# Kernel tuning notes

Measured on AMD Instinct MI355X. Metric: run time of the kernel, lower is better.

The kernel has to match this reference:

```python
import jax, jax.numpy as jnp
import numpy as np

N_LAYERS = 6
D_T = 6144   # d_transcoder (features per layer)
D_M = 768    # d_model (residual stream)
TOK = 128    # tokens (batch*seq)


def setup_inputs() -> dict:
    key = jax.random.key(0)
    k_x, k_enc, k_dec = jax.random.split(key, 3)
    x = jax.random.normal(k_x, (N_LAYERS, TOK, D_M), jnp.float32)
    W_enc = jax.random.normal(k_enc, (N_LAYERS, D_T, D_M), jnp.float32) * 0.02
    b_enc = jnp.zeros((N_LAYERS, D_T), jnp.float32)
    b_dec = jnp.zeros((N_LAYERS, D_M), jnp.float32)
    # Padded cross-layer decoder: W_dec[i, j] is the decoder from features at
    # layer i writing into layer j's MLP output; only j >= i is valid
    # (original stores a ragged list of [d_transcoder, n_layers - i, d_model]).
    W_dec = jax.random.normal(k_dec, (N_LAYERS, N_LAYERS, D_T, D_M), jnp.float32) * 0.02
    dec_mask = jnp.triu(jnp.ones((N_LAYERS, N_LAYERS), dtype=bool))  # mask[i, j] = (j >= i)
    W_dec = jnp.where(dec_mask[:, :, None, None], W_dec, 0.0)
    return {"x": x, "W_enc": W_enc, "b_enc": b_enc, "b_dec": b_dec,
            "W_dec": W_dec, "dec_mask": dec_mask}


def reference(x, W_enc, b_enc, b_dec, W_dec, dec_mask):
    # Encode: per-layer feature activations [n_layers, tok, d_transcoder]
    acts = jax.nn.relu(jnp.einsum('lnd,lfd->lnf', x, W_enc) + b_enc[:, None, :])
    # Decode: layer-i features write to all layers j >= i (mask enforces triangle)
    Wd = jnp.where(dec_mask[:, :, None, None], W_dec, 0.0)
    recon = jnp.einsum('inf,ijfd->jnd', acts, Wd) + b_dec[:, None, :]
    return recon  # [n_layers, tok, d_model]
```

## Files before the change

kernel.cpp:

```cpp
#include <hip/hip_runtime.h>
#include <hip/hip_bf16.h>

#define NL 6
#define DT 6144
#define DM 768
#define TOK 128

#define EF 32
#define EK 256
#define ENST (DM / EK)

#define TD 256
#define NTD 3
#define FC 768
#define NFC 8
#define NSTEP (FC / 32)
#define TILE_ELEMS (TOK * TD)

#define FCA 384
#define NFCA 16
#define NSTEPA (FCA / 32)

using bf16x8 = __attribute__((ext_vector_type(8))) short;
using f32x4  = __attribute__((ext_vector_type(4))) float;

typedef unsigned int u32;
typedef __attribute__((address_space(1))) const u32 gu32;
typedef __attribute__((address_space(3))) u32 lu32;

__device__ __forceinline__ void stage16(const float* g, float* l) {
  __builtin_amdgcn_global_load_lds((gu32*)g, (lu32*)l, 16, 0, 0);
}

__device__ __forceinline__ short f2bf(float f) {
  union { float f; unsigned u; } c; c.f = f;
  unsigned u = c.u;
  u += 0x7fffu + ((u >> 16) & 1u);
  return (short)(u >> 16);
}

__global__ void initcvt_k(const float* __restrict__ b_dec,
                          const float* __restrict__ x,
                          float* __restrict__ out, ushort* __restrict__ xb) {
  int idx = blockIdx.x * 256 + threadIdx.x;
  if (idx < NL * TOK * DM) {
    out[idx] = b_dec[(idx / (TOK * DM)) * DM + (idx % DM)];
    xb[idx] = (ushort)f2bf(x[idx]);
  }
}

__global__ __launch_bounds__(256, 2) void encode_k(
    const ushort* __restrict__ xb, const float* __restrict__ W_enc,
    const float* __restrict__ b_enc, ushort* __restrict__ acts)
{
  __shared__ float lw[2][EF][EK];

  const int l  = blockIdx.x / (DT / EF);
  const int f0 = (blockIdx.x % (DT / EF)) * EF;
  const int w    = threadIdx.x >> 6;
  const int lane = threadIdx.x & 63;
  const int lo = lane & 15, hi = lane >> 4;

  const float*  We = W_enc + ((size_t)l * DT + f0) * DM;
  const ushort* Xb = xb + (size_t)l * TOK * DM;

  f32x4 acc[2][2];
  #pragma unroll
  for (int mi = 0; mi < 2; ++mi)
    #pragma unroll
    for (int ni = 0; ni < 2; ++ni)
      acc[mi][ni] = f32x4{0.f, 0.f, 0.f, 0.f};

  #pragma unroll
  for (int q = 0; q < 8; ++q) {
    const int row = w * 8 + q;
    const int g   = lane ^ (row & 7);
    stage16(We + (size_t)row * DM + g * 4, &lw[0][row][0]);
  }
  __syncthreads();

  int cur = 0;
  #pragma unroll 1
  for (int st = 0; st < ENST; ++st) {
    if (st + 1 < ENST) {
      #pragma unroll
      for (int q = 0; q < 8; ++q) {
        const int row = w * 8 + q;
        const int g   = lane ^ (row & 7);
        stage16(We + (size_t)row * DM + (st + 1) * EK + g * 4,
                &lw[cur ^ 1][row][0]);
      }
    }

    const int sw = lo & 7;
    #pragma unroll
    for (int ks = 0; ks < EK / 32; ++ks) {
      bf16x8 a[2], b[2];
      #pragma unroll
      for (int mi = 0; mi < 2; ++mi)
        a[mi] = *(const bf16x8*)(Xb + (size_t)(w * 32 + mi * 16 + lo) * DM
                                 + st * EK + ks * 32 + hi * 8);
      #pragma unroll
      for (int ni = 0; ni < 2; ++ni) {
        const int c0 = (ks * 8 + hi * 2) ^ sw;
        const int c1 = (ks * 8 + hi * 2 + 1) ^ sw;
        const float4 b0 = *(const float4*)&lw[cur][ni * 16 + lo][c0 * 4];
        const float4 b1 = *(const float4*)&lw[cur][ni * 16 + lo][c1 * 4];
        b[ni][0] = f2bf(b0.x); b[ni][1] = f2bf(b0.y);
        b[ni][2] = f2bf(b0.z); b[ni][3] = f2bf(b0.w);
        b[ni][4] = f2bf(b1.x); b[ni][5] = f2bf(b1.y);
        b[ni][6] = f2bf(b1.z); b[ni][7] = f2bf(b1.w);
      }

      #pragma unroll
      for (int mi = 0; mi < 2; ++mi)
        #pragma unroll
        for (int ni = 0; ni < 2; ++ni)
          acc[mi][ni] = __builtin_amdgcn_mfma_f32_16x16x32_bf16(a[mi], b[ni], acc[mi][ni], 0, 0, 0);
    }

    __syncthreads();
    cur ^= 1;
  }

  #pragma unroll
  for (int ni = 0; ni < 2; ++ni) {
    const int f = f0 + ni * 16 + lo;
    const float bias = b_enc[l * DT + f];
    #pragma unroll
    for (int mi = 0; mi < 2; ++mi) {
      #pragma unroll
      for (int rr = 0; rr < 4; ++rr) {
        const int n = w * 32 + mi * 16 + hi * 4 + rr;
        float v = acc[mi][ni][rr] + bias;
        v = v > 0.f ? v : 0.f;
        acts[((size_t)l * TOK + n) * DT + f] = (ushort)f2bf(v);
      }
    }
  }
}

__device__ const int PI_[21]  = {0,0,0,0,0,0, 1,1,1,1,1, 2,2,2,2, 3,3,3, 4,4, 5};
__device__ const int PJ_[21]  = {0,1,2,3,4,5, 1,2,3,4,5, 2,3,4,5, 3,4,5, 4,5, 5};
__device__ const int OFFI_[6] = {0, 6, 11, 15, 18, 20};

__global__ __launch_bounds__(256, 2) void decode_part_k(
    const ushort* __restrict__ acts, const float* __restrict__ W_dec,
    float* __restrict__ part)
{
  __shared__ float lw[2][32][TD];

  const int bid = blockIdx.x;
  const int p  = bid / (NTD * NFC);
  const int rm = bid % (NTD * NFC);
  const int c  = rm / NTD;
  const int t  = rm % NTD;
  const int i = PI_[p], j = PJ_[p];
  const int w = threadIdx.x >> 6;
  const int lane = threadIdx.x & 63;
  const int lo = lane & 15, hi = lane >> 4;
  const int fb = c * FC;

  const float*  Wb = W_dec + ((size_t)(i * NL + j) * DT + fb) * DM + t * TD;
  const ushort* Ab = acts + (size_t)i * TOK * DT + fb;

  f32x4 acc[8][4];
  #pragma unroll
  for (int mi = 0; mi < 8; ++mi)
    #pragma unroll
    for (int ni = 0; ni < 4; ++ni)
      acc[mi][ni] = f32x4{0.f, 0.f, 0.f, 0.f};

  #pragma unroll
  for (int q = 0; q < 8; ++q) {
    const int row = w * 8 + q;
    stage16(Wb + (size_t)row * DM + lane * 4, &lw[0][row][0]);
  }
  __syncthreads();

  int cur = 0;
  #pragma unroll 1
  for (int s = 0; s < NSTEP; ++s) {
    if (s + 1 < NSTEP) {
      const float* Ws = Wb + (size_t)(s + 1) * 32 * DM;
      #pragma unroll
      for (int q = 0; q < 8; ++q) {
        const int row = w * 8 + q;
        stage16(Ws + (size_t)row * DM + lane * 4, &lw[cur ^ 1][row][0]);
      }
    }

    bf16x8 a[8];
    #pragma unroll
    for (int mi = 0; mi < 8; ++mi)
      a[mi] = *(const bf16x8*)(Ab + (size_t)(mi * 16 + lo) * DT + s * 32 + hi * 8);

    bf16x8 bb[4];
    #pragma unroll
    for (int ni = 0; ni < 4; ++ni) {
      const int col = w * 64 + ni * 16 + lo;
      #pragma unroll
      for (int e = 0; e < 8; ++e)
        bb[ni][e] = f2bf(lw[cur][hi * 8 + e][col]);
    }

    #pragma unroll
    for (int mi = 0; mi < 8; ++mi)
      #pragma unroll
      for (int ni = 0; ni < 4; ++ni)
        acc[mi][ni] = __builtin_amdgcn_mfma_f32_16x16x32_bf16(a[mi], bb[ni], acc[mi][ni], 0, 0, 0);

    __syncthreads();
    cur ^= 1;
  }

  float* pp = part + (size_t)bid * TILE_ELEMS;
  #pragma unroll
  for (int ni = 0; ni < 4; ++ni) {
    const int dl = w * 64 + ni * 16 + lo;
    #pragma unroll
    for (int mi = 0; mi < 8; ++mi)
      #pragma unroll
      for (int rr = 0; rr < 4; ++rr)
        pp[(size_t)(mi * 16 + hi * 4 + rr) * TD + dl] = acc[mi][ni][rr];
  }
}

__global__ void reduce_k(const float* __restrict__ part,
                         const float* __restrict__ b_dec,
                         float* __restrict__ out)
{
  const int idx = blockIdx.x * 256 + threadIdx.x;
  if (idx >= NL * TOK * DM) return;
  const int j   = idx / (TOK * DM);
  const int rem = idx % (TOK * DM);
  const int n   = rem / DM;
  const int d   = rem % DM;
  const int t   = d >> 8;
  const int dl  = d & (TD - 1);

  float s = b_dec[j * DM + d];
  for (int i = 0; i <= j; ++i) {
    const int p = OFFI_[i] + (j - i);
    const float* pb = part + ((size_t)(p * NFC) * NTD + t) * TILE_ELEMS
                      + (size_t)n * TD + dl;
    #pragma unroll
    for (int c = 0; c < NFC; ++c)
      s += pb[(size_t)c * NTD * TILE_ELEMS];
  }
  out[idx] = s;
}

__global__ __launch_bounds__(256, 2) void decode_atomic_k(
    const ushort* __restrict__ acts, const float* __restrict__ W_dec,
    float* __restrict__ out)
{
  __shared__ float lw[2][32][TD];

  const int bid = blockIdx.x;
  const int p  = bid / (NTD * NFCA);
  const int rm = bid % (NTD * NFCA);
  const int c  = rm / NTD;
  const int t  = rm % NTD;
  const int i = PI_[p], j = PJ_[p];
  const int w = threadIdx.x >> 6;
  const int lane = threadIdx.x & 63;
  const int lo = lane & 15, hi = lane >> 4;
  const int fb = c * FCA;

  const float*  Wb = W_dec + ((size_t)(i * NL + j) * DT + fb) * DM + t * TD;
  const ushort* Ab = acts + (size_t)i * TOK * DT + fb;

  f32x4 acc[8][4];
  #pragma unroll
  for (int mi = 0; mi < 8; ++mi)
    #pragma unroll
    for (int ni = 0; ni < 4; ++ni)
      acc[mi][ni] = f32x4{0.f, 0.f, 0.f, 0.f};

  #pragma unroll
  for (int q = 0; q < 8; ++q) {
    const int row = w * 8 + q;
    stage16(Wb + (size_t)row * DM + lane * 4, &lw[0][row][0]);
  }
  __syncthreads();

  int cur = 0;
  #pragma unroll 1
  for (int s = 0; s < NSTEPA; ++s) {
    if (s + 1 < NSTEPA) {
      const float* Ws = Wb + (size_t)(s + 1) * 32 * DM;
      #pragma unroll
      for (int q = 0; q < 8; ++q) {
        const int row = w * 8 + q;
        stage16(Ws + (size_t)row * DM + lane * 4, &lw[cur ^ 1][row][0]);
      }
    }

    bf16x8 a[8];
    #pragma unroll
    for (int mi = 0; mi < 8; ++mi)
      a[mi] = *(const bf16x8*)(Ab + (size_t)(mi * 16 + lo) * DT + s * 32 + hi * 8);

    bf16x8 bb[4];
    #pragma unroll
    for (int ni = 0; ni < 4; ++ni) {
      const int col = w * 64 + ni * 16 + lo;
      #pragma unroll
      for (int e = 0; e < 8; ++e)
        bb[ni][e] = f2bf(lw[cur][hi * 8 + e][col]);
    }

    #pragma unroll
    for (int mi = 0; mi < 8; ++mi)
      #pragma unroll
      for (int ni = 0; ni < 4; ++ni)
        acc[mi][ni] = __builtin_amdgcn_mfma_f32_16x16x32_bf16(a[mi], bb[ni], acc[mi][ni], 0, 0, 0);

    __syncthreads();
    cur ^= 1;
  }

  float* oj = out + (size_t)j * TOK * DM;
  #pragma unroll
  for (int ni = 0; ni < 4; ++ni) {
    const int d = t * TD + w * 64 + ni * 16 + lo;
    #pragma unroll
    for (int mi = 0; mi < 8; ++mi)
      #pragma unroll
      for (int rr = 0; rr < 4; ++rr)
        atomicAdd(oj + (size_t)(mi * 16 + hi * 4 + rr) * DM + d, acc[mi][ni][rr]);
  }
}

extern "C" void kernel_launch(void* const* d_in, const int* in_sizes, int n_in,
                              void* d_out, int out_size, void* d_ws, size_t ws_size,
                              hipStream_t stream) {
  const float* x     = (const float*)d_in[0];
  const float* W_enc = (const float*)d_in[1];
  const float* b_enc = (const float*)d_in[2];
  const float* b_dec = (const float*)d_in[3];
  const float* W_dec = (const float*)d_in[4];
  float* out = (float*)d_out;

  const size_t actsB = (size_t)NL * TOK * DT * 2;
  const size_t xbB   = (size_t)NL * TOK * DM * 2;
  const size_t partB = (size_t)21 * NFC * NTD * TILE_ELEMS * 4;

  ushort* acts = (ushort*)d_ws;
  ushort* xb   = (ushort*)((char*)d_ws + actsB);
  float*  part = (float*)((char*)d_ws + actsB + xbB);

  initcvt_k<<<dim3((NL * TOK * DM + 255) / 256), dim3(256), 0, stream>>>(b_dec, x, out, xb);
  encode_k<<<dim3(NL * (DT / EF)), dim3(256), 0, stream>>>(xb, W_enc, b_enc, acts);

  if (ws_size >= actsB + xbB + partB) {
    decode_part_k<<<dim3(21 * NFC * NTD), dim3(256), 0, stream>>>(acts, W_dec, part);
    reduce_k<<<dim3((NL * TOK * DM + 255) / 256), dim3(256), 0, stream>>>(part, b_dec, out);
  } else {
    decode_atomic_k<<<dim3(21 * NFCA * NTD), dim3(256), 0, stream>>>(acts, W_dec, out);
  }
}
```

Measured before the change: 185.1 us.

## Store decode partials in bf16, remap blocks per XCD, double encode tile per block

Decode partial sums are now written and read as bf16 instead of fp32, halving the partial buffer traffic between decode_part_k and reduce_k. Decode blocks are remapped so that consecutive logical tiles land on the same XCD (8 XCDs × 63), aiming for better L2 locality of shared acts. Each encode block now handles two 32-feature tiles in sequence (grid shrinks to NL*96), with the pipelined staging continuing across tiles. The bf16 partials lose precision in the reduction, with up to 48 partials summed per output.

```diff
diff --git a/kernel.cpp b/kernel.cpp
--- a/kernel.cpp
+++ b/kernel.cpp
@@ -9,6 +9,7 @@
 #define EF 32
 #define EK 256
 #define ENST (DM / EK)
+#define NVE (2 * ENST)
 
 #define TD 256
 #define NTD 3
@@ -37,6 +38,11 @@
   unsigned u = c.u;
   u += 0x7fffu + ((u >> 16) & 1u);
   return (short)(u >> 16);
+}
+
+__device__ __forceinline__ float bf2f(ushort u) {
+  union { unsigned u; float f; } c; c.u = ((unsigned)u) << 16;
+  return c.f;
 }
 
 __global__ void initcvt_k(const float* __restrict__ b_dec,
@@ -55,13 +61,13 @@
 {
   __shared__ float lw[2][EF][EK];
 
-  const int l  = blockIdx.x / (DT / EF);
-  const int f0 = (blockIdx.x % (DT / EF)) * EF;
+  const int l  = blockIdx.x / 96;
+  const int fp = (blockIdx.x % 96) * 64;
   const int w    = threadIdx.x >> 6;
   const int lane = threadIdx.x & 63;
   const int lo = lane & 15, hi = lane >> 4;
 
-  const float*  We = W_enc + ((size_t)l * DT + f0) * DM;
+  const float*  We = W_enc + ((size_t)l * DT + fp) * DM;
   const ushort* Xb = xb + (size_t)l * TOK * DM;
 
   f32x4 acc[2][2];
@@ -74,20 +80,23 @@
   #pragma unroll
   for (int q = 0; q < 8; ++q) {
     const int row = w * 8 + q;
-    const int g   = lane ^ (row & 7);
-    stage16(We + (size_t)row * DM + g * 4, &lw[0][row][0]);
+    stage16(We + (size_t)row * DM + (lane ^ (row & 7)) * 4, &lw[0][row][0]);
   }
   __syncthreads();
 
   int cur = 0;
   #pragma unroll 1
-  for (int st = 0; st < ENST; ++st) {
-    if (st + 1 < ENST) {
+  for (int v = 0; v < NVE; ++v) {
+    const int tt = v / ENST;
+    const int st = v % ENST;
+
+    if (v + 1 < NVE) {
+      const int tt2 = (v + 1) / ENST;
+      const int st2 = (v + 1) % ENST;
       #pragma unroll
       for (int q = 0; q < 8; ++q) {
         const int row = w * 8 + q;
-        const int g   = lane ^ (row & 7);
-        stage16(We + (size_t)row * DM + (st + 1) * EK + g * 4,
+        stage16(We + (size_t)(tt2 * EF + row) * DM + st2 * EK + (lane ^ (row & 7)) * 4,
                 &lw[cur ^ 1][row][0]);
       }
     }
@@ -119,24 +128,27 @@
           acc[mi][ni] = __builtin_amdgcn_mfma_f32_16x16x32_bf16(a[mi], b[ni], acc[mi][ni], 0, 0, 0);
     }
 
+    if (st == ENST - 1) {
+      #pragma unroll
+      for (int ni = 0; ni < 2; ++ni) {
+        const int f = fp + tt * EF + ni * 16 + lo;
+        const float bias = b_enc[l * DT + f];
+        #pragma unroll
+        for (int mi = 0; mi < 2; ++mi) {
+          #pragma unroll
+          for (int rr = 0; rr < 4; ++rr) {
+            const int n = w * 32 + mi * 16 + hi * 4 + rr;
+            float vv = acc[mi][ni][rr] + bias;
+            vv = vv > 0.f ? vv : 0.f;
+            acts[((size_t)l * TOK + n) * DT + f] = (ushort)f2bf(vv);
+            acc[mi][ni][rr] = 0.f;
+          }
+        }
+      }
+    }
+
     __syncthreads();
     cur ^= 1;
-  }
-
-  #pragma unroll
-  for (int ni = 0; ni < 2; ++ni) {
-    const int f = f0 + ni * 16 + lo;
-    const float bias = b_enc[l * DT + f];
-    #pragma unroll
-    for (int mi = 0; mi < 2; ++mi) {
-      #pragma unroll
-      for (int rr = 0; rr < 4; ++rr) {
-        const int n = w * 32 + mi * 16 + hi * 4 + rr;
-        float v = acc[mi][ni][rr] + bias;
-        v = v > 0.f ? v : 0.f;
-        acts[((size_t)l * TOK + n) * DT + f] = (ushort)f2bf(v);
-      }
-    }
   }
 }
 
@@ -146,13 +158,15 @@
 
 __global__ __launch_bounds__(256, 2) void decode_part_k(
     const ushort* __restrict__ acts, const float* __restrict__ W_dec,
-    float* __restrict__ part)
+    ushort* __restrict__ part)
 {
   __shared__ float lw[2][32][TD];
 
-  const int bid = blockIdx.x;
-  const int p  = bid / (NTD * NFC);
-  const int rm = bid % (NTD * NFC);
+  const int xcd = blockIdx.x & 7;
+  const int idx = blockIdx.x >> 3;
+  const int logical = xcd * 63 + idx;
+  const int p  = logical / (NFC * NTD);
+  const int rm = logical % (NFC * NTD);
   const int c  = rm / NTD;
   const int t  = rm % NTD;
   const int i = PI_[p], j = PJ_[p];
@@ -160,6 +174,7 @@
   const int lane = threadIdx.x & 63;
   const int lo = lane & 15, hi = lane >> 4;
   const int fb = c * FC;
+  (void)j;
 
   const float*  Wb = W_dec + ((size_t)(i * NL + j) * DT + fb) * DM + t * TD;
   const ushort* Ab = acts + (size_t)i * TOK * DT + fb;
@@ -214,7 +229,7 @@
     cur ^= 1;
   }
 
-  float* pp = part + (size_t)bid * TILE_ELEMS;
+  ushort* pp = part + (size_t)logical * TILE_ELEMS;
   #pragma unroll
   for (int ni = 0; ni < 4; ++ni) {
     const int dl = w * 64 + ni * 16 + lo;
@@ -222,11 +237,11 @@
     for (int mi = 0; mi < 8; ++mi)
       #pragma unroll
       for (int rr = 0; rr < 4; ++rr)
-        pp[(size_t)(mi * 16 + hi * 4 + rr) * TD + dl] = acc[mi][ni][rr];
-  }
-}
-
-__global__ void reduce_k(const float* __restrict__ part,
+        pp[(size_t)(mi * 16 + hi * 4 + rr) * TD + dl] = (ushort)f2bf(acc[mi][ni][rr]);
+  }
+}
+
+__global__ void reduce_k(const ushort* __restrict__ part,
                          const float* __restrict__ b_dec,
                          float* __restrict__ out)
 {
@@ -242,11 +257,11 @@
   float s = b_dec[j * DM + d];
   for (int i = 0; i <= j; ++i) {
     const int p = OFFI_[i] + (j - i);
-    const float* pb = part + ((size_t)(p * NFC) * NTD + t) * TILE_ELEMS
-                      + (size_t)n * TD + dl;
+    const ushort* pb = part + ((size_t)(p * NFC) * NTD + t) * TILE_ELEMS
+                       + (size_t)n * TD + dl;
     #pragma unroll
     for (int c = 0; c < NFC; ++c)
-      s += pb[(size_t)c * NTD * TILE_ELEMS];
+      s += bf2f(pb[(size_t)c * NTD * TILE_ELEMS]);
   }
   out[idx] = s;
 }
@@ -345,14 +360,14 @@
 
   const size_t actsB = (size_t)NL * TOK * DT * 2;
   const size_t xbB   = (size_t)NL * TOK * DM * 2;
-  const size_t partB = (size_t)21 * NFC * NTD * TILE_ELEMS * 4;
+  const size_t partB = (size_t)21 * NFC * NTD * TILE_ELEMS * 2;
 
   ushort* acts = (ushort*)d_ws;
   ushort* xb   = (ushort*)((char*)d_ws + actsB);
-  float*  part = (float*)((char*)d_ws + actsB + xbB);
+  ushort* part = (ushort*)((char*)d_ws + actsB + xbB);
 
   initcvt_k<<<dim3((NL * TOK * DM + 255) / 256), dim3(256), 0, stream>>>(b_dec, x, out, xb);
-  encode_k<<<dim3(NL * (DT / EF)), dim3(256), 0, stream>>>(xb, W_enc, b_enc, acts);
+  encode_k<<<dim3(NL * 96), dim3(256), 0, stream>>>(xb, W_enc, b_enc, acts);
 
   if (ws_size >= actsB + xbB + partB) {
     decode_part_k<<<dim3(21 * NFC * NTD), dim3(256), 0, stream>>>(acts, W_dec, part);
```

New measurement: 187.8 us. About the same (+1.5%).
